# Optimization experiments

Hardware: AMD Instinct MI355X
Metric: run time of the kernel (lower is better)

Reference implementation:

```python
import jax, jax.numpy as jnp
import numpy as np

D_MODEL = 1024
NHEAD = 16
HEAD_DIM = D_MODEL // NHEAD


def setup_inputs() -> dict:
    key = jax.random.key(0)
    k1, k2, k3 = jax.random.split(key, 3)
    x = jax.random.normal(k1, (4, 2048, D_MODEL), dtype=jnp.float32)
    # xavier_uniform init for weights, zero bias
    lim_qkv = float(np.sqrt(6.0 / (D_MODEL + 3 * D_MODEL)))
    w_qkv = jax.random.uniform(k2, (3 * D_MODEL, D_MODEL), jnp.float32, -lim_qkv, lim_qkv)
    b_qkv = jnp.zeros((3 * D_MODEL,), jnp.float32)
    lim_o = float(np.sqrt(6.0 / (D_MODEL + D_MODEL)))
    w_o = jax.random.uniform(k3, (D_MODEL, D_MODEL), jnp.float32, -lim_o, lim_o)
    b_o = jnp.zeros((D_MODEL,), jnp.float32)
    return {"x": x, "w_qkv": w_qkv, "b_qkv": b_qkv, "w_o": w_o, "b_o": b_o}


def reference(x, w_qkv, b_qkv, w_o, b_o):
    B, S, _ = x.shape
    qkv = x @ w_qkv.T + b_qkv                      # [B,S,3D]
    qkv = qkv.reshape(B, S, NHEAD, 3 * HEAD_DIM).transpose(0, 2, 1, 3)  # [B,H,S,3d]
    q, k, v = jnp.split(qkv, 3, axis=-1)           # each [B,H,S,d]
    scale = 1.0 / jnp.sqrt(jnp.asarray(HEAD_DIM, x.dtype))
    logits = jnp.einsum('bhqd,bhkd->bhqk', q, k) * scale
    attn = jax.nn.softmax(logits, axis=-1)
    vals = jnp.einsum('bhqk,bhkd->bhqd', attn, v)  # [B,H,S,d]
    vals = vals.transpose(0, 2, 1, 3).reshape(B, S, D_MODEL)
    return vals @ w_o.T + b_o
```

## Files before the change

kernel.cpp:

```cpp
#include <hip/hip_runtime.h>
#include <hip/hip_bf16.h>
#include <stdint.h>

typedef unsigned short u16;
typedef uint32_t u32;
typedef __bf16 bf16x8 __attribute__((ext_vector_type(8)));
typedef __bf16 bf16x2v __attribute__((ext_vector_type(2)));
typedef float f32x2 __attribute__((ext_vector_type(2)));
typedef float f32x4 __attribute__((ext_vector_type(4)));
typedef float f32x16 __attribute__((ext_vector_type(16)));
typedef u16 u16x4v __attribute__((ext_vector_type(4)));
typedef u32 u32x2 __attribute__((ext_vector_type(2)));

#define AS1 __attribute__((address_space(1)))
#define AS3 __attribute__((address_space(3)))

__device__ __forceinline__ void gld_lds16(const u16* g, u16* l) {
    __builtin_amdgcn_global_load_lds((const AS1 uint32_t*)g, (AS3 uint32_t*)l, 16, 0, 0);
}

__device__ __forceinline__ u16 f2bf(float f) {
    union { float f; uint32_t u; } v; v.f = f;
    uint32_t u = v.u;
    return (u16)((u + 0x7FFFu + ((u >> 16) & 1u)) >> 16);
}

__device__ __forceinline__ u32 pkbf16(float lo, float hi) {
    f32x2 e; e[0] = lo; e[1] = hi;
    union { bf16x2v b; u32 d; } u;
    u.b = __builtin_convertvector(e, bf16x2v);
    return u.d;
}

__device__ __forceinline__ u32x2 pl32swap(u32 a, u32 b) {
#if __has_builtin(__builtin_amdgcn_permlane32_swap)
    return __builtin_amdgcn_permlane32_swap(a, b, false, false);
#else
    asm volatile("v_permlane32_swap_b32 %0, %1" : "+v"(a), "+v"(b));
    u32x2 r; r[0] = a; r[1] = b; return r;
#endif
}

__device__ __forceinline__ void smpack(const f32x16& sv, f32x2& la,
                                       bf16x8& A0v, bf16x8& A1v) {
    u32 pk[8];
#pragma unroll
    for (int p = 0; p < 8; ++p) {
        const float e0 = __builtin_amdgcn_exp2f(sv[2 * p]);
        const float e1 = __builtin_amdgcn_exp2f(sv[2 * p + 1]);
        f32x2 e2; e2[0] = e0; e2[1] = e1;
        la += e2;
        pk[p] = pkbf16(e0, e1);
    }
    const u32x2 r02 = pl32swap(pk[0], pk[2]);
    const u32x2 r13 = pl32swap(pk[1], pk[3]);
    const u32x2 r46 = pl32swap(pk[4], pk[6]);
    const u32x2 r57 = pl32swap(pk[5], pk[7]);
    union { u32 d[4]; bf16x8 v; } A0, A1;
    A0.d[0] = r02[0]; A0.d[1] = r13[0]; A0.d[2] = r02[1]; A0.d[3] = r13[1];
    A1.d[0] = r46[0]; A1.d[1] = r57[0]; A1.d[2] = r46[1]; A1.d[3] = r57[1];
    A0v = A0.v; A1v = A1.v;
}

#define QSCALE 0.18033688011112042f

__global__ void cast_all(const float* __restrict__ x, const float* __restrict__ wq,
                         const float* __restrict__ wo, u16* __restrict__ xb,
                         u16* __restrict__ wqb, u16* __restrict__ wob) {
    const int i = blockIdx.x * blockDim.x + threadIdx.x;
    const float* in; u16* out; int j;
    if (i < 2097152)      { in = x;  out = xb;  j = i; }
    else if (i < 2883584) { in = wq; out = wqb; j = i - 2097152; }
    else                  { in = wo; out = wob; j = i - 2883584; }
    float4 f = ((const float4*)in)[j];
    u16x4v o;
    o.x = f2bf(f.x); o.y = f2bf(f.y); o.z = f2bf(f.z); o.w = f2bf(f.w);
    ((u16x4v*)out)[j] = o;
}

template <int MODE>
__global__ __launch_bounds__(256, 3) void gemm_bt(
    const u16* __restrict__ A, const u16* __restrict__ B,
    const float* __restrict__ bias, float* __restrict__ Cf,
    u16* __restrict__ qb, u16* __restrict__ kb, u16* __restrict__ vT,
    int K, int ldc)
{
    __shared__ __align__(16) u16 As[128 * 64];
    __shared__ __align__(16) u16 Bs[128 * 64];
    const int tid = threadIdx.x;
    const int lane = tid & 63;
    const int w = tid >> 6;
    const int wm = (w >> 1) << 6;
    const int wn = (w & 1) << 6;
    const int r = lane & 15;
    const int q = lane >> 4;

    const int nwgx = gridDim.x;
    const int flat = blockIdx.y * nwgx + blockIdx.x;
    const int cpx = (nwgx * gridDim.y) >> 3;
    const int swz = (flat & 7) * cpx + (flat >> 3);
    const int m0 = (swz / nwgx) << 7;
    const int n0 = (swz % nwgx) << 7;

    const f32x4 zero4 = {0.f, 0.f, 0.f, 0.f};
    f32x4 acc[4][4];
#pragma unroll
    for (int i = 0; i < 4; ++i)
#pragma unroll
        for (int j = 0; j < 4; ++j) acc[i][j] = zero4;

    const int nk = K >> 6;
    for (int kt = 0; kt < nk; ++kt) {
        const int kk = kt << 6;
#pragma unroll
        for (int p = 0; p < 4; ++p) {
            const int idx = (p << 8) + tid;
            const int row = idx >> 3;
            const int cg = ((idx & 7) - row) & 7;
            gld_lds16(A + (m0 + row) * K + kk + (cg << 3), &As[idx << 3]);
            gld_lds16(B + (n0 + row) * K + kk + (cg << 3), &Bs[idx << 3]);
        }
        __syncthreads();
#pragma unroll
        for (int s = 0; s < 2; ++s) {
            bf16x8 af[4], bf[4];
#pragma unroll
            for (int i = 0; i < 4; ++i) {
                const int ra = wm + (i << 4) + r;
                af[i] = *(const bf16x8*)&As[(ra << 6) + ((((s << 2) + q + ra) & 7) << 3)];
                const int rb = wn + (i << 4) + r;
                bf[i] = *(const bf16x8*)&Bs[(rb << 6) + ((((s << 2) + q + rb) & 7) << 3)];
            }
#pragma unroll
            for (int i = 0; i < 4; ++i)
#pragma unroll
                for (int j = 0; j < 4; ++j)
                    acc[i][j] = __builtin_amdgcn_mfma_f32_16x16x32_bf16(af[i], bf[j], acc[i][j], 0, 0, 0);
        }
        __syncthreads();
    }

#pragma unroll
    for (int j = 0; j < 4; ++j) {
        const int col = n0 + wn + (j << 4) + r;
        const float bv = bias[col];
        if (MODE == 0) {
#pragma unroll
            for (int i = 0; i < 4; ++i)
#pragma unroll
                for (int ii = 0; ii < 4; ++ii) {
                    const int rowg = m0 + wm + (i << 4) + (q << 2) + ii;
                    Cf[rowg * ldc + col] = acc[i][j][ii] + bv;
                }
        } else {
            const int c0 = n0 + wn + (j << 4);
            const int h = c0 / 192;
            const int rem = c0 - h * 192;
            const int region = rem >> 6;
            const int colp = (h << 6) + (rem - (region << 6)) + r;
            if (region == 0) {
#pragma unroll
                for (int i = 0; i < 4; ++i)
#pragma unroll
                    for (int ii = 0; ii < 4; ++ii) {
                        const int rowg = m0 + wm + (i << 4) + (q << 2) + ii;
                        qb[rowg * 1024 + colp] = f2bf((acc[i][j][ii] + bv) * QSCALE);
                    }
            } else if (region == 1) {
#pragma unroll
                for (int i = 0; i < 4; ++i)
#pragma unroll
                    for (int ii = 0; ii < 4; ++ii) {
                        const int rowg = m0 + wm + (i << 4) + (q << 2) + ii;
                        kb[rowg * 1024 + colp] = f2bf(acc[i][j][ii] + bv);
                    }
            } else {
#pragma unroll
                for (int i = 0; i < 4; ++i) {
                    const int rowg0 = m0 + wm + (i << 4) + (q << 2);
                    u16x4v vv;
                    vv.x = f2bf(acc[i][j][0] + bv);
                    vv.y = f2bf(acc[i][j][1] + bv);
                    vv.z = f2bf(acc[i][j][2] + bv);
                    vv.w = f2bf(acc[i][j][3] + bv);
                    *(u16x4v*)&vT[(size_t)colp * 8192 + rowg0] = vv;
                }
            }
        }
    }
}

__global__ __launch_bounds__(256, 2) void attn(
    const u16* __restrict__ qb, const u16* __restrict__ kb,
    const u16* __restrict__ vT, u16* __restrict__ vals)
{
    __shared__ __align__(16) u16 S[16384];

    const int tid  = threadIdx.x;
    const int lane = tid & 63;
    const int w    = tid >> 6;
    const int c    = lane & 31;
    const int h2   = lane >> 5;
    const int head = blockIdx.x;
    const int q0   = blockIdx.y << 8;
    const int b    = blockIdx.z;
    const size_t rowbase = (size_t)b * 2048;

#pragma unroll
    for (int p = 0; p < 8; ++p) {
        const int idx = (p << 8) + tid;
        const int row = idx >> 3;
        const int cg  = ((idx & 7) - row) & 7;
        gld_lds16(qb + (rowbase + q0 + row) * 1024 + (head << 6) + (cg << 3), &S[idx << 3]);
    }
    __syncthreads();

    bf16x8 bq[4][2];
#pragma unroll
    for (int nt = 0; nt < 2; ++nt) {
        const int qr = (w << 6) + (nt << 5) + c;
#pragma unroll
        for (int dc = 0; dc < 4; ++dc)
            bq[dc][nt] = *(const bf16x8*)&S[(qr << 6) + ((((dc << 1) + h2 + qr) & 7) << 3)];
    }
    __syncthreads();

    const int srow8 = tid >> 3;
    const int scg   = ((tid & 7) - srow8) & 7;
    const u16* gK = kb + (rowbase + srow8) * 1024 + (head << 6) + (scg << 3);
    const u16* gV = vT + (size_t)((head << 6) + srow8) * 8192 + rowbase + (scg << 3);

    {
        u16* buf = S + 8192;
        gld_lds16(gK,             &buf[tid << 3]);
        gld_lds16(gK + 32 * 1024, &buf[2048 + (tid << 3)]);
        gld_lds16(gV,             &buf[4096 + (tid << 3)]);
        gld_lds16(gV + 32 * 8192, &buf[6144 + (tid << 3)]);
    }
    __syncthreads();

    int aF[4];
#pragma unroll
    for (int i = 0; i < 4; ++i)
        aF[i] = (c << 6) + ((((i << 1) + h2 + c) & 7) << 3);

    const int mtw = w & 1;
    int aK[2][4];
    int aV[2][4];
#pragma unroll
    for (int i = 0; i < 4; ++i) {
        const int a0 = aF[i];
        const int a1 = aF[i] + 2048;
        aK[0][i] = mtw ? a1 : a0;
        aK[1][i] = mtw ? a0 : a1;
    }
#pragma unroll
    for (int ht = 0; ht < 2; ++ht)
#pragma unroll
        for (int c16 = 0; c16 < 2; ++c16) {
            const int i = (ht << 1) | c16;
            const int v0 = aF[c16] + (ht << 11);
            const int v1 = aF[2 + c16] + (ht << 11);
            aV[0][i] = mtw ? v1 : v0;
            aV[1][i] = mtw ? v0 : v1;
        }

    f32x16 oacc[2][2];
    f32x2 la2[2];
    f32x16 zero16;
#pragma unroll
    for (int i = 0; i < 16; ++i) {
        zero16[i] = 0.f;
        oacc[0][0][i] = 0.f; oacc[0][1][i] = 0.f;
        oacc[1][0][i] = 0.f; oacc[1][1][i] = 0.f;
    }
    la2[0][0] = 0.f; la2[0][1] = 0.f;
    la2[1][0] = 0.f; la2[1][1] = 0.f;

    const u16* gKr = gK + 65536;
    const u16* gVr = gV + 64;

    for (int kt = 0; kt < 32; ++kt) {
        const int cur = kt & 1;
        if (kt > 0) __syncthreads();
        u16* bufP = (cur == 0) ? (S + 0) : (S + 8192);
        const u16* bufC = (cur == 0) ? (S + 8192) : (S + 0);
        if (kt < 31) {
            gld_lds16(gKr,             &bufP[tid << 3]);
            gld_lds16(gKr + 32 * 1024, &bufP[2048 + (tid << 3)]);
            gld_lds16(gVr,             &bufP[4096 + (tid << 3)]);
            gld_lds16(gVr + 32 * 8192, &bufP[6144 + (tid << 3)]);
            gKr += 65536;
            gVr += 64;
        }
        const u16* Ks  = bufC;
        const u16* VTs = bufC + 4096;

#pragma unroll
        for (int mm = 0; mm < 2; ++mm) {
            __builtin_amdgcn_s_setprio(1);
            const bf16x8 ak0 = *(const bf16x8*)&Ks[aK[mm][0]];
            f32x16 s0 = __builtin_amdgcn_mfma_f32_32x32x16_bf16(ak0, bq[0][0], zero16, 0, 0, 0);
            f32x16 s1 = __builtin_amdgcn_mfma_f32_32x32x16_bf16(ak0, bq[0][1], zero16, 0, 0, 0);
#pragma unroll
            for (int dc = 1; dc < 4; ++dc) {
                const bf16x8 ak = *(const bf16x8*)&Ks[aK[mm][dc]];
                s0 = __builtin_amdgcn_mfma_f32_32x32x16_bf16(ak, bq[dc][0], s0, 0, 0, 0);
                s1 = __builtin_amdgcn_mfma_f32_32x32x16_bf16(ak, bq[dc][1], s1, 0, 0, 0);
            }
            __builtin_amdgcn_s_setprio(0);

            bf16x8 av[4];
#pragma unroll
            for (int i = 0; i < 4; ++i)
                av[i] = *(const bf16x8*)&VTs[aV[mm][i]];

#pragma unroll
            for (int nt = 0; nt < 2; ++nt) {
                const f32x16& sv = (nt == 0) ? s0 : s1;
                bf16x8 A0v, A1v;
                smpack(sv, la2[nt], A0v, A1v);

                __builtin_amdgcn_s_setprio(1);
#pragma unroll
                for (int ht = 0; ht < 2; ++ht) {
                    oacc[ht][nt] = __builtin_amdgcn_mfma_f32_32x32x16_bf16(av[(ht << 1) | 0], A0v, oacc[ht][nt], 0, 0, 0);
                    oacc[ht][nt] = __builtin_amdgcn_mfma_f32_32x32x16_bf16(av[(ht << 1) | 1], A1v, oacc[ht][nt], 0, 0, 0);
                }
                __builtin_amdgcn_s_setprio(0);
            }
        }
    }

#pragma unroll
    for (int nt = 0; nt < 2; ++nt) {
        float myl = la2[nt][0] + la2[nt][1];
        myl += __shfl_xor(myl, 32, 64);
        const float inv = 1.f / myl;
        const size_t orow = rowbase + q0 + (w << 6) + (nt << 5) + c;
#pragma unroll
        for (int ht = 0; ht < 2; ++ht)
#pragma unroll
            for (int r4 = 0; r4 < 4; ++r4) {
                u16x4v vv;
                vv.x = f2bf(oacc[ht][nt][4 * r4 + 0] * inv);
                vv.y = f2bf(oacc[ht][nt][4 * r4 + 1] * inv);
                vv.z = f2bf(oacc[ht][nt][4 * r4 + 2] * inv);
                vv.w = f2bf(oacc[ht][nt][4 * r4 + 3] * inv);
                const int hd0 = (ht << 5) + (r4 << 3) + (h2 << 2);
                *(u16x4v*)&vals[orow * 1024 + (head << 6) + hd0] = vv;
            }
    }
}

extern "C" void kernel_launch(void* const* d_in, const int* in_sizes, int n_in,
                              void* d_out, int out_size, void* d_ws, size_t ws_size,
                              hipStream_t stream) {
    (void)in_sizes; (void)n_in; (void)out_size; (void)ws_size;
    const float* x     = (const float*)d_in[0];
    const float* w_qkv = (const float*)d_in[1];
    const float* b_qkv = (const float*)d_in[2];
    const float* w_o   = (const float*)d_in[3];
    const float* b_o   = (const float*)d_in[4];
    float* out = (float*)d_out;

    char* ws = (char*)d_ws;
    u16* xb    = (u16*)(ws);
    u16* wqkvb = (u16*)(ws + (size_t)(16 << 20));
    u16* wob   = (u16*)(ws + (size_t)(22 << 20));
    u16* qb    = (u16*)(ws + (size_t)(24 << 20));
    u16* kb    = (u16*)(ws + (size_t)(40 << 20));
    u16* vTb   = (u16*)(ws + (size_t)(56 << 20));
    u16* valsb = (u16*)(ws + (size_t)(72 << 20));

    cast_all<<<12288, 256, 0, stream>>>(x, w_qkv, w_o, xb, wqkvb, wob);

    gemm_bt<1><<<dim3(24, 64), 256, 0, stream>>>(xb, wqkvb, b_qkv, nullptr,
                                                 qb, kb, vTb, 1024, 3072);

    attn<<<dim3(16, 8, 4), 256, 0, stream>>>(qb, kb, vTb, valsb);

    gemm_bt<0><<<dim3(8, 64), 256, 0, stream>>>(valsb, wob, b_o, out,
                                                nullptr, nullptr, nullptr, 1024, 1024);
}
```

Measured before the change: 243.1 us.

## Double-buffer GEMM LDS tiles with async prefetch of next K-slice

Splits the GEMM shared-memory tiles into two 32-wide K buffers and prefetches the next slice via global_load_lds while MFMAs run on the current one. Explicit vmcnt waits and raw barriers replace __syncthreads, so load latency can overlap compute. The K step is halved, which doubles the barrier count and changes the LDS swizzle pattern. Correctness depends on the vmcnt(4) count matching the number of outstanding loads.

```diff
diff --git a/kernel.cpp b/kernel.cpp
--- a/kernel.cpp
+++ b/kernel.cpp
@@ -85,8 +85,8 @@
     u16* __restrict__ qb, u16* __restrict__ kb, u16* __restrict__ vT,
     int K, int ldc)
 {
-    __shared__ __align__(16) u16 As[128 * 64];
-    __shared__ __align__(16) u16 Bs[128 * 64];
+    __shared__ __align__(16) u16 As[2][128 * 32];
+    __shared__ __align__(16) u16 Bs[2][128 * 32];
     const int tid = threadIdx.x;
     const int lane = tid & 63;
     const int w = tid >> 6;
@@ -109,35 +109,52 @@
 #pragma unroll
         for (int j = 0; j < 4; ++j) acc[i][j] = zero4;
 
-    const int nk = K >> 6;
+    const int nk = K >> 5;
+
+#pragma unroll
+    for (int p = 0; p < 2; ++p) {
+        const int idx = (p << 8) + tid;
+        const int row = idx >> 2;
+        const int cg = ((idx & 3) - (row >> 1)) & 3;
+        gld_lds16(A + (m0 + row) * K + (cg << 3), &As[0][idx << 3]);
+        gld_lds16(B + (n0 + row) * K + (cg << 3), &Bs[0][idx << 3]);
+    }
+
     for (int kt = 0; kt < nk; ++kt) {
-        const int kk = kt << 6;
-#pragma unroll
-        for (int p = 0; p < 4; ++p) {
-            const int idx = (p << 8) + tid;
-            const int row = idx >> 3;
-            const int cg = ((idx & 7) - row) & 7;
-            gld_lds16(A + (m0 + row) * K + kk + (cg << 3), &As[idx << 3]);
-            gld_lds16(B + (n0 + row) * K + kk + (cg << 3), &Bs[idx << 3]);
-        }
-        __syncthreads();
-#pragma unroll
-        for (int s = 0; s < 2; ++s) {
-            bf16x8 af[4], bf[4];
-#pragma unroll
-            for (int i = 0; i < 4; ++i) {
-                const int ra = wm + (i << 4) + r;
-                af[i] = *(const bf16x8*)&As[(ra << 6) + ((((s << 2) + q + ra) & 7) << 3)];
-                const int rb = wn + (i << 4) + r;
-                bf[i] = *(const bf16x8*)&Bs[(rb << 6) + ((((s << 2) + q + rb) & 7) << 3)];
+        const int cur = kt & 1;
+        if (kt + 1 < nk) {
+            const int kk = (kt + 1) << 5;
+#pragma unroll
+            for (int p = 0; p < 2; ++p) {
+                const int idx = (p << 8) + tid;
+                const int row = idx >> 2;
+                const int cg = ((idx & 3) - (row >> 1)) & 3;
+                gld_lds16(A + (m0 + row) * K + kk + (cg << 3), &As[cur ^ 1][idx << 3]);
+                gld_lds16(B + (n0 + row) * K + kk + (cg << 3), &Bs[cur ^ 1][idx << 3]);
             }
-#pragma unroll
-            for (int i = 0; i < 4; ++i)
-#pragma unroll
-                for (int j = 0; j < 4; ++j)
-                    acc[i][j] = __builtin_amdgcn_mfma_f32_16x16x32_bf16(af[i], bf[j], acc[i][j], 0, 0, 0);
-        }
-        __syncthreads();
+            asm volatile("s_waitcnt vmcnt(4)" ::: "memory");
+        } else {
+            asm volatile("s_waitcnt vmcnt(0)" ::: "memory");
+        }
+        __builtin_amdgcn_s_barrier();
+        asm volatile("" ::: "memory");
+
+        bf16x8 af[4], bf[4];
+#pragma unroll
+        for (int i = 0; i < 4; ++i) {
+            const int ra = wm + (i << 4) + r;
+            af[i] = *(const bf16x8*)&As[cur][((ra << 2) + ((q + (ra >> 1)) & 3)) << 3];
+            const int rb = wn + (i << 4) + r;
+            bf[i] = *(const bf16x8*)&Bs[cur][((rb << 2) + ((q + (rb >> 1)) & 3)) << 3];
+        }
+#pragma unroll
+        for (int i = 0; i < 4; ++i)
+#pragma unroll
+            for (int j = 0; j < 4; ++j)
+                acc[i][j] = __builtin_amdgcn_mfma_f32_16x16x32_bf16(af[i], bf[j], acc[i][j], 0, 0, 0);
+
+        asm volatile("" ::: "memory");
+        __builtin_amdgcn_s_barrier();
     }
 
 #pragma unroll
```

Measured after the change: 256.6 us. 5.6% more time.
